# Kernel tuning notes

Hardware: AMD Instinct MI355X
Metric: run time of the kernel (lower is better)

Reference implementation:

```python
import jax, jax.numpy as jnp
import numpy as np

N_HEAD = 16
G_HEADS = 2
D_HEAD = 64
D_MODEL = 1024
HEAD_RATIO = N_HEAD // G_HEADS  # 8
QK_DIM = G_HEADS * D_HEAD       # 128
SCALE = 1.0 / D_HEAD ** 0.5
LN_EPS = 1e-5


def _rel_shift(x):
    # x: [qlen, rlen, B, n] -- Transformer-XL relative shift
    q, r = x.shape[0], x.shape[1]
    x_pad = jnp.pad(x, ((0, 0), (1, 0), (0, 0), (0, 0)))      # [q, r+1, B, n]
    x_pad = x_pad.reshape(r + 1, q, *x.shape[2:])[1:]          # drop first row
    return x_pad.reshape(q, r, *x.shape[2:])


def setup_inputs() -> dict:
    key = jax.random.key(0)
    ks = jax.random.split(key, 9)
    qlen, bsz, levels = 1024, 4, 3
    w = jax.random.normal(ks[0], (qlen, bsz, D_MODEL), jnp.float32)
    r = jax.random.normal(ks[1], (qlen, D_MODEL), jnp.float32)
    r_w_bias = jax.random.normal(ks[2], (G_HEADS, D_HEAD), jnp.float32) * 0.02
    r_r_bias = jax.random.normal(ks[3], (G_HEADS, D_HEAD), jnp.float32) * 0.02
    masks = jax.random.uniform(ks[4], (qlen, qlen, levels), jnp.float32)
    W_qkv = jax.random.normal(ks[5], (2 * QK_DIM + N_HEAD * D_HEAD, D_MODEL), jnp.float32) * 0.02
    W_r = jax.random.normal(ks[6], (QK_DIM, D_MODEL), jnp.float32) * 0.02
    mask_proj = jnp.ones((levels, N_HEAD), jnp.float32)
    W_o = jax.random.normal(ks[7], (D_MODEL, N_HEAD * D_HEAD), jnp.float32) * 0.02
    ln_gamma = jnp.ones((D_MODEL,), jnp.float32)
    ln_beta = jnp.zeros((D_MODEL,), jnp.float32)
    return dict(w=w, r=r, r_w_bias=r_w_bias, r_r_bias=r_r_bias, masks=masks,
                W_qkv=W_qkv, W_r=W_r, mask_proj=mask_proj, W_o=W_o,
                ln_gamma=ln_gamma, ln_beta=ln_beta)


def reference(w, r, r_w_bias, r_r_bias, masks, W_qkv, W_r, mask_proj, W_o, ln_gamma, ln_beta):
    qlen, bsz, _ = w.shape
    rlen = r.shape[0]
    N = qlen  # no mems: klen == qlen == rlen

    w_heads = w @ W_qkv.T                                   # [q, B, 1280]
    r_head_k = (r @ W_r.T).reshape(rlen, G_HEADS, D_HEAD)   # [r, gH, d]
    w_head_q = w_heads[..., :QK_DIM].reshape(qlen, bsz, G_HEADS, D_HEAD)
    w_head_k = w_heads[..., QK_DIM:2 * QK_DIM].reshape(qlen, bsz, G_HEADS, D_HEAD)
    w_head_v = w_heads[..., 2 * QK_DIM:].reshape(qlen, bsz, N_HEAD, D_HEAD)

    AC = jnp.einsum('ibnd,jbnd->ijbn', w_head_q + r_w_bias, w_head_k)
    BD = jnp.einsum('ibnd,jnd->ijbn', w_head_q + r_r_bias, r_head_k)
    BD = _rel_shift(BD)
    attn_score = (AC + BD) * SCALE                           # [N, N, B, gH]

    # per-head mask mixing ('full' projection)
    attn = jnp.transpose(attn_score, (2, 3, 0, 1))           # [B, gH, N, N]
    mw = (masks @ mask_proj).reshape(N, N, G_HEADS, HEAD_RATIO)
    mw = jnp.transpose(mw, (2, 0, 1, 3))                     # [gH, N, N, hr]
    attn = attn[..., None] * mw[None]                        # [B, gH, N, N, hr]
    attn = jnp.transpose(attn, (0, 1, 4, 2, 3)).reshape(bsz, N_HEAD, N, N)
    attn_score = jnp.transpose(attn, (2, 3, 0, 1))           # [N, N, B, H]

    attn_prob = jax.nn.softmax(attn_score, axis=1)
    attn_vec = jnp.einsum('ijbn,jbnd->ibnd', attn_prob, w_head_v)
    attn_vec = attn_vec.reshape(qlen, bsz, N_HEAD * D_HEAD)
    attn_out = attn_vec @ W_o.T                              # [q, B, d_model]

    # post-LN residual
    x = w + attn_out
    mu = jnp.mean(x, axis=-1, keepdims=True)
    var = jnp.mean((x - mu) ** 2, axis=-1, keepdims=True)
    return (x - mu) * jax.lax.rsqrt(var + LN_EPS) * ln_gamma + ln_beta
```

## Files before the change

### kernel.cpp

```cpp
#include <hip/hip_runtime.h>
#include <cstddef>
#include <cstdint>

#define QLEN   1024
#define SCALE  0.125f
#define LN_EPS 1e-5f
#define DMODEL 1024

typedef __bf16 bf16x8 __attribute__((ext_vector_type(8)));
typedef __bf16 bf16x4 __attribute__((ext_vector_type(4)));
typedef float  f32x4  __attribute__((ext_vector_type(4)));

__device__ __forceinline__ void load16_lds(const void* g, void* l) {
  __builtin_amdgcn_global_load_lds(
      (const __attribute__((address_space(1))) unsigned int*)g,
      (__attribute__((address_space(3))) unsigned int*)l, 16, 0, 0);
}

__device__ __forceinline__ void bar_lds() {
  asm volatile("s_waitcnt lgkmcnt(0)" ::: "memory");
  __builtin_amdgcn_s_barrier();
  asm volatile("" ::: "memory");
}

__global__ __launch_bounds__(256) void cast_all(
    const float* __restrict__ w, __bf16* __restrict__ w_bf,
    const float* __restrict__ Wqkv, __bf16* __restrict__ Wqkv_bf,
    const float* __restrict__ r, __bf16* __restrict__ r_bf,
    const float* __restrict__ Wr, __bf16* __restrict__ Wr_bf,
    const float* __restrict__ Wo, __bf16* __restrict__ Wo_bf)
{
  int blk = blockIdx.x;
  const float* in; __bf16* out;
  if (blk < 2048)      { in = w;    out = w_bf;    }
  else if (blk < 2688) { blk -= 2048; in = Wqkv; out = Wqkv_bf; }
  else if (blk < 3200) { blk -= 2688; in = r;    out = r_bf;    }
  else if (blk < 3264) { blk -= 3200; in = Wr;   out = Wr_bf;   }
  else                 { blk -= 3264; in = Wo;   out = Wo_bf;   }
  const size_t i = ((size_t)blk * 256 + threadIdx.x) * 8;
  const float4 a = *(const float4*)&in[i];
  const float4 b = *(const float4*)&in[i + 4];
  bf16x8 o;
  o[0] = (__bf16)a.x; o[1] = (__bf16)a.y; o[2] = (__bf16)a.z; o[3] = (__bf16)a.w;
  o[4] = (__bf16)b.x; o[5] = (__bf16)b.y; o[6] = (__bf16)b.z; o[7] = (__bf16)b.w;
  *(bf16x8*)&out[i] = o;
}

__global__ __launch_bounds__(256) void gemm_proj(
    const __bf16* __restrict__ w_bf, const __bf16* __restrict__ Wqkv_bf,
    const __bf16* __restrict__ r_bf, const __bf16* __restrict__ Wr_bf,
    const float* __restrict__ rwb, const float* __restrict__ rrb,
    __bf16* __restrict__ Qw, __bf16* __restrict__ Qr,
    __bf16* __restrict__ Kb, __bf16* __restrict__ Vt,
    __bf16* __restrict__ Rb)
{
  __shared__ __bf16 Asl[128 * 64];
  __shared__ __bf16 Bsl[64 * 64];
  const int blk = blockIdx.x;
  const bool isR = blk >= 640;
  const __bf16 *A, *B;
  int m0, n0;
  if (!isR) { A = w_bf; B = Wqkv_bf; n0 = (blk % 20) * 64; m0 = (blk / 20) * 128; }
  else      { const int k = blk - 640; A = r_bf; B = Wr_bf;
              n0 = (k % 2) * 64; m0 = (k / 2) * 128; }

  const int tid = threadIdx.x, lane = tid & 63, wv = tid >> 6;
  const int lr = lane & 15, kq = lane >> 4;
  const int s = lane & 7, ar = lane >> 3;

  f32x4 acc[2][4];
#pragma unroll
  for (int mt = 0; mt < 2; ++mt)
#pragma unroll
    for (int nt = 0; nt < 4; ++nt)
      acc[mt][nt] = (f32x4){0.f, 0.f, 0.f, 0.f};

  for (int k0 = 0; k0 < 1024; k0 += 64) {
#pragma unroll
    for (int p = 0; p < 4; ++p) {
      const int row = wv * 32 + p * 8 + ar;
      const int gc = (s - (row & 7)) & 7;
      load16_lds(A + (size_t)(m0 + row) * 1024 + k0 + gc * 8,
                 &Asl[row * 64 + s * 8]);
    }
#pragma unroll
    for (int p = 0; p < 2; ++p) {
      const int row = wv * 16 + p * 8 + ar;
      const int gc = (s - (row & 7)) & 7;
      load16_lds(B + (size_t)(n0 + row) * 1024 + k0 + gc * 8,
                 &Bsl[row * 64 + s * 8]);
    }
    __syncthreads();
#pragma unroll
    for (int ks = 0; ks < 2; ++ks) {
      const int c = ks * 4 + kq;
      bf16x8 af[2], bfr[4];
#pragma unroll
      for (int mt = 0; mt < 2; ++mt) {
        const int row = wv * 32 + mt * 16 + lr;
        af[mt] = *(const bf16x8*)&Asl[row * 64 + ((c + (row & 7)) & 7) * 8];
      }
#pragma unroll
      for (int nt = 0; nt < 4; ++nt) {
        const int row = nt * 16 + lr;
        bfr[nt] = *(const bf16x8*)&Bsl[row * 64 + ((c + (row & 7)) & 7) * 8];
      }
#pragma unroll
      for (int mt = 0; mt < 2; ++mt)
#pragma unroll
        for (int nt = 0; nt < 4; ++nt)
          acc[mt][nt] = __builtin_amdgcn_mfma_f32_16x16x32_bf16(
              af[mt], bfr[nt], acc[mt][nt], 0, 0, 0);
    }
    __syncthreads();
  }

#pragma unroll
  for (int mt = 0; mt < 2; ++mt) {
    const int row0 = m0 + wv * 32 + mt * 16 + kq * 4;
#pragma unroll
    for (int nt = 0; nt < 4; ++nt) {
      const int gcol = n0 + nt * 16 + lr;
      const f32x4 c = acc[mt][nt];
      if (isR) {
        const int g = gcol >> 6, d = gcol & 63;
#pragma unroll
        for (int reg = 0; reg < 4; ++reg)
          Rb[(size_t)g * 65536 + (size_t)(row0 + reg) * 64 + d] = (__bf16)c[reg];
      } else if (gcol < 128) {
        const int g = gcol >> 6, d = gcol & 63;
        const float bw = rwb[gcol], br = rrb[gcol];
#pragma unroll
        for (int reg = 0; reg < 4; ++reg) {
          const int row = row0 + reg, i = row >> 2, b = row & 3;
          const size_t o = (size_t)(b * 2 + g) * 65536 + (size_t)i * 64 + d;
          Qw[o] = (__bf16)(c[reg] + bw);
          Qr[o] = (__bf16)(c[reg] + br);
        }
      } else if (gcol < 256) {
        const int lc = gcol - 128, g = lc >> 6, d = lc & 63;
#pragma unroll
        for (int reg = 0; reg < 4; ++reg) {
          const int row = row0 + reg, i = row >> 2, b = row & 3;
          Kb[(size_t)(b * 2 + g) * 65536 + (size_t)i * 64 + d] = (__bf16)c[reg];
        }
      } else {
        const int lc = gcol - 256, h = lc >> 6, d = lc & 63;
#pragma unroll
        for (int reg = 0; reg < 4; ++reg) {
          const int row = row0 + reg, i = row >> 2, b = row & 3;
          Vt[((size_t)((b * 16 + h) * 64 + d)) * 1024 + i] = (__bf16)c[reg];
        }
      }
    }
  }
}

__global__ __launch_bounds__(256) void gemm_wo(
    const __bf16* __restrict__ A, const __bf16* __restrict__ B,
    float* __restrict__ C0, float* __restrict__ C1)
{
  __shared__ __bf16 Asl[128 * 64];
  __shared__ __bf16 Bsl[64 * 64];
  const int m0 = blockIdx.y * 128, n0 = blockIdx.x * 64;
  const int kh = blockIdx.z;
  float* __restrict__ C = kh ? C1 : C0;
  const int tid = threadIdx.x, lane = tid & 63, wv = tid >> 6;
  const int lr = lane & 15, kq = lane >> 4;
  const int s = lane & 7, ar = lane >> 3;
  const int kbase = kh * 512;

  f32x4 acc[2][4];
#pragma unroll
  for (int mt = 0; mt < 2; ++mt)
#pragma unroll
    for (int nt = 0; nt < 4; ++nt)
      acc[mt][nt] = (f32x4){0.f, 0.f, 0.f, 0.f};

  for (int k0 = 0; k0 < 512; k0 += 64) {
#pragma unroll
    for (int p = 0; p < 4; ++p) {
      const int row = wv * 32 + p * 8 + ar;
      const int gc = (s - (row & 7)) & 7;
      load16_lds(A + (size_t)(m0 + row) * 1024 + kbase + k0 + gc * 8,
                 &Asl[row * 64 + s * 8]);
    }
#pragma unroll
    for (int p = 0; p < 2; ++p) {
      const int row = wv * 16 + p * 8 + ar;
      const int gc = (s - (row & 7)) & 7;
      load16_lds(B + (size_t)(n0 + row) * 1024 + kbase + k0 + gc * 8,
                 &Bsl[row * 64 + s * 8]);
    }
    __syncthreads();
#pragma unroll
    for (int ks = 0; ks < 2; ++ks) {
      const int c = ks * 4 + kq;
      bf16x8 af[2], bfr[4];
#pragma unroll
      for (int mt = 0; mt < 2; ++mt) {
        const int row = wv * 32 + mt * 16 + lr;
        af[mt] = *(const bf16x8*)&Asl[row * 64 + ((c + (row & 7)) & 7) * 8];
      }
#pragma unroll
      for (int nt = 0; nt < 4; ++nt) {
        const int row = nt * 16 + lr;
        bfr[nt] = *(const bf16x8*)&Bsl[row * 64 + ((c + (row & 7)) & 7) * 8];
      }
#pragma unroll
      for (int mt = 0; mt < 2; ++mt)
#pragma unroll
        for (int nt = 0; nt < 4; ++nt)
          acc[mt][nt] = __builtin_amdgcn_mfma_f32_16x16x32_bf16(
              af[mt], bfr[nt], acc[mt][nt], 0, 0, 0);
    }
    __syncthreads();
  }

#pragma unroll
  for (int mt = 0; mt < 2; ++mt) {
    const int row0 = m0 + wv * 32 + mt * 16 + kq * 4;
#pragma unroll
    for (int nt = 0; nt < 4; ++nt) {
      const int col = n0 + nt * 16 + lr;
      const f32x4 c = acc[mt][nt];
#pragma unroll
      for (int reg = 0; reg < 4; ++reg)
        C[(size_t)(row0 + reg) * 1024 + col] = c[reg];
    }
  }
}

__global__ __launch_bounds__(256) void gemm64_bf16(
    const __bf16* __restrict__ Qw, const __bf16* __restrict__ Qr,
    const __bf16* __restrict__ Kb, const __bf16* __restrict__ Rb,
    __bf16* __restrict__ AC, __bf16* __restrict__ BDo)
{
  __shared__ __bf16 Asl[128 * 64];
  __shared__ __bf16 Bsl[128 * 64];
  const int tid = threadIdx.x, lane = tid & 63, wv = tid >> 6;
  const int which = blockIdx.z & 1, bat = blockIdx.z >> 1;
  const int m0 = blockIdx.y * 128, n0 = blockIdx.x * 128;
  const __bf16* Ap = (which ? Qr : Qw) + (size_t)bat * 65536;
  const __bf16* Bp = which ? (Rb + (size_t)(bat & 1) * 65536)
                           : (Kb + (size_t)bat * 65536);
  __bf16* Cp = (which ? BDo : AC) + (size_t)bat * 1048576;

#pragma unroll
  for (int p = 0; p < 4; ++p) {
    const int row = wv * 32 + p * 8 + (lane >> 3);
    const int s = lane & 7;
    const int gc = (s - (row & 7)) & 7;
    load16_lds(Ap + (size_t)(m0 + row) * 64 + gc * 8, &Asl[row * 64 + s * 8]);
    load16_lds(Bp + (size_t)(n0 + row) * 64 + gc * 8, &Bsl[row * 64 + s * 8]);
  }
  __syncthreads();

  const int lr = lane & 15, kq = lane >> 4;
  const int wm = (wv >> 1) * 64, wn = (wv & 1) * 64;
  f32x4 acc[4][4];
#pragma unroll
  for (int mt = 0; mt < 4; ++mt)
#pragma unroll
    for (int nt = 0; nt < 4; ++nt)
      acc[mt][nt] = (f32x4){0.f, 0.f, 0.f, 0.f};

#pragma unroll
  for (int ks = 0; ks < 2; ++ks) {
    const int c = ks * 4 + kq;
    bf16x8 af[4], bfr[4];
#pragma unroll
    for (int mt = 0; mt < 4; ++mt) {
      const int row = wm + mt * 16 + lr;
      af[mt] = *(const bf16x8*)&Asl[row * 64 + ((c + (row & 7)) & 7) * 8];
    }
#pragma unroll
    for (int nt = 0; nt < 4; ++nt) {
      const int row = wn + nt * 16 + lr;
      bfr[nt] = *(const bf16x8*)&Bsl[row * 64 + ((c + (row & 7)) & 7) * 8];
    }
#pragma unroll
    for (int mt = 0; mt < 4; ++mt)
#pragma unroll
      for (int nt = 0; nt < 4; ++nt)
        acc[mt][nt] = __builtin_amdgcn_mfma_f32_16x16x32_bf16(
            af[mt], bfr[nt], acc[mt][nt], 0, 0, 0);
  }

#pragma unroll
  for (int mt = 0; mt < 4; ++mt) {
    const int row0 = m0 + wm + mt * 16 + kq * 4;
#pragma unroll
    for (int nt = 0; nt < 4; ++nt) {
      const int col = n0 + wn + nt * 16 + lr;
      const f32x4 cc = acc[mt][nt];
      if (which) {
#pragma unroll
        for (int reg = 0; reg < 4; ++reg) {
          const int k = row0 + reg;
          const int thr = 1023 - k;
          if (col >= thr) {
            Cp[(size_t)k * 1024 + (col - thr)] = (__bf16)cc[reg];
            if (col == thr && k < 1023)
              Cp[(size_t)k * 1024 + (k + 1)] = (__bf16)0.f;
          } else if (k > 0) {
            Cp[(size_t)(k - 1) * 1024 + (col + k + 1)] = (__bf16)cc[reg];
          }
        }
      } else {
#pragma unroll
        for (int reg = 0; reg < 4; ++reg)
          Cp[(size_t)(row0 + reg) * 1024 + col] = (__bf16)cc[reg];
      }
    }
  }
}

__global__ __launch_bounds__(256) void prep3(
    const __bf16* __restrict__ AC, const __bf16* __restrict__ BDs,
    __bf16* __restrict__ Tg,
    const float* __restrict__ masks, const float* __restrict__ mproj,
    __bf16* __restrict__ Mh)
{
  const int tid = threadIdx.x;
  if (blockIdx.x < 2048) {
    const size_t base = (size_t)blockIdx.x * 4096 + (size_t)tid * 16;
    const bf16x8 a0 = *(const bf16x8*)&AC[base];
    const bf16x8 a1 = *(const bf16x8*)&AC[base + 8];
    const bf16x8 b0 = *(const bf16x8*)&BDs[base];
    const bf16x8 b1 = *(const bf16x8*)&BDs[base + 8];
    bf16x8 o0, o1;
#pragma unroll
    for (int k = 0; k < 8; ++k) {
      o0[k] = (__bf16)(((float)a0[k] + (float)b0[k]) * SCALE);
      o1[k] = (__bf16)(((float)a1[k] + (float)b1[k]) * SCALE);
    }
    *(bf16x8*)&Tg[base] = o0;
    *(bf16x8*)&Tg[base + 8] = o1;
  } else {
    const int blk = blockIdx.x - 2048;
    const size_t ij0 = ((size_t)blk * 256 + tid) * 4;
    const float4 a = *(const float4*)&masks[ij0 * 3];
    const float4 b = *(const float4*)&masks[ij0 * 3 + 4];
    const float4 c = *(const float4*)&masks[ij0 * 3 + 8];
    const float m0[4] = {a.x, a.w, b.z, c.y};
    const float m1[4] = {a.y, b.x, b.w, c.z};
    const float m2[4] = {a.z, b.y, c.x, c.w};
#pragma unroll
    for (int h = 0; h < 16; ++h) {
      const float p0 = mproj[h], p1 = mproj[16 + h], p2 = mproj[32 + h];
      bf16x4 o;
#pragma unroll
      for (int k = 0; k < 4; ++k)
        o[k] = (__bf16)(m0[k] * p0 + m1[k] * p1 + m2[k] * p2);
      *(bf16x4*)&Mh[(size_t)h * 1048576 + ij0] = o;
    }
  }
}

__global__ __launch_bounds__(256, 6) void attn10(
    const __bf16* __restrict__ Tg, const __bf16* __restrict__ Mh,
    const __bf16* __restrict__ Vt, __bf16* __restrict__ av, const int b0)
{
  __shared__ __bf16 P[2][32 * 128];
  __shared__ float rinvS[32];
  const int tid = threadIdx.x;
  const int i0 = blockIdx.x * 32;
  const int h = blockIdx.y, b = blockIdx.z + b0;
  const int g = h >> 3;
  const size_t bg = (size_t)(b * 2 + g);
  const int r = tid >> 3, li = tid & 7;
  const __bf16* Trow = Tg + bg * 1048576 + (size_t)(i0 + r) * 1024 + li * 8;
  const __bf16* Mrow = Mh + (size_t)h * 1048576 + (size_t)(i0 + r) * 1024 + li * 8;

  const int lane = tid & 63, wv = tid >> 6;
  const int m = lane & 15, kq = lane >> 4;
  const __bf16* vbase = Vt + ((size_t)((b * 16 + h) * 64 + wv * 16 + m)) * 1024 + kq * 8;

  float sum = 0.f;
  f32x4 acc[2][2];
#pragma unroll
  for (int mt = 0; mt < 2; ++mt)
#pragma unroll
    for (int u = 0; u < 2; ++u)
      acc[mt][u] = (f32x4){0.f, 0.f, 0.f, 0.f};

  bf16x8 t[2], mk[2], v[4];
#pragma unroll
  for (int q = 0; q < 2; ++q) {
    t[q]  = *(const bf16x8*)&Trow[q * 64];
    mk[q] = *(const bf16x8*)&Mrow[q * 64];
  }

  for (int ch = 0; ch < 8; ++ch) {
    const int cb = ch & 1;
#pragma unroll
    for (int ks = 0; ks < 4; ++ks)
      v[ks] = *(const bf16x8*)&vbase[(ch * 4 + ks) * 32];
#pragma unroll
    for (int q = 0; q < 2; ++q) {
      bf16x8 p8;
      float s0 = 0.f;
#pragma unroll
      for (int k = 0; k < 8; ++k) {
        const float e = __expf((float)t[q][k] * (float)mk[q][k]);
        s0 += e;
        p8[k] = (__bf16)e;
      }
      sum += s0;
      const int slot = (q * 8 + li) ^ (r & 7);
      *(bf16x8*)&P[cb][r * 128 + slot * 8] = p8;
    }
    if (ch < 7) {
#pragma unroll
      for (int q = 0; q < 2; ++q) {
        t[q]  = *(const bf16x8*)&Trow[(ch + 1) * 128 + q * 64];
        mk[q] = *(const bf16x8*)&Mrow[(ch + 1) * 128 + q * 64];
      }
    }
    bar_lds();
    __builtin_amdgcn_s_setprio(1);
#pragma unroll
    for (int ks = 0; ks < 4; ++ks) {
      const int c = ks * 4 + kq;
#pragma unroll
      for (int mt = 0; mt < 2; ++mt) {
        const int R = mt * 16 + m;
        const bf16x8 a = *(const bf16x8*)&P[cb][R * 128 + ((c ^ (R & 7)) << 3)];
        acc[mt][ks & 1] = __builtin_amdgcn_mfma_f32_16x16x32_bf16(
            a, v[ks], acc[mt][ks & 1], 0, 0, 0);
      }
    }
    __builtin_amdgcn_s_setprio(0);
  }

  sum += __shfl_xor(sum, 1);
  sum += __shfl_xor(sum, 2);
  sum += __shfl_xor(sum, 4);
  if (li == 0) rinvS[r] = 1.f / sum;
  __syncthreads();

#pragma unroll
  for (int mt = 0; mt < 2; ++mt) {
    const f32x4 accf = acc[mt][0] + acc[mt][1];
#pragma unroll
    for (int reg = 0; reg < 4; ++reg) {
      const int row = mt * 16 + kq * 4 + reg;
      av[((size_t)(i0 + row) * 4 + b) * 1024 + h * 64 + wv * 16 + m] =
          (__bf16)(accf[reg] * rinvS[row]);
    }
  }
}

__global__ __launch_bounds__(256) void ln_kernel(
    const float* __restrict__ w, const float* __restrict__ ao0,
    const float* __restrict__ ao1,
    const float* __restrict__ gamma, const float* __restrict__ beta,
    float* __restrict__ out)
{
  const int tid = threadIdx.x;
  const int lane = tid & 63, wv = tid >> 6;
  const size_t base = (size_t)blockIdx.x * DMODEL + tid * 4;
  __shared__ float red[8];
  const float4 xw = *(const float4*)&w[base];
  const float4 xa = *(const float4*)&ao0[base];
  const float4 xb = *(const float4*)&ao1[base];
  float x[4] = {xw.x + xa.x + xb.x, xw.y + xa.y + xb.y,
                xw.z + xa.z + xb.z, xw.w + xa.w + xb.w};
  float s = (x[0] + x[1]) + (x[2] + x[3]);
  s += __shfl_xor(s, 1);  s += __shfl_xor(s, 2);  s += __shfl_xor(s, 4);
  s += __shfl_xor(s, 8);  s += __shfl_xor(s, 16); s += __shfl_xor(s, 32);
  if (lane == 0) red[wv] = s;
  __syncthreads();
  const float mu = (red[0] + red[1] + red[2] + red[3]) * (1.f / DMODEL);
  float s2 = 0.f;
#pragma unroll
  for (int p = 0; p < 4; ++p) { const float t = x[p] - mu; s2 += t * t; }
  s2 += __shfl_xor(s2, 1);  s2 += __shfl_xor(s2, 2);  s2 += __shfl_xor(s2, 4);
  s2 += __shfl_xor(s2, 8);  s2 += __shfl_xor(s2, 16); s2 += __shfl_xor(s2, 32);
  if (lane == 0) red[4 + wv] = s2;
  __syncthreads();
  const float rs = rsqrtf((red[4] + red[5] + red[6] + red[7]) * (1.f / DMODEL) + LN_EPS);
  const float4 g4 = *(const float4*)&gamma[tid * 4];
  const float4 b4 = *(const float4*)&beta[tid * 4];
  float4 o;
  o.x = (x[0] - mu) * rs * g4.x + b4.x;
  o.y = (x[1] - mu) * rs * g4.y + b4.y;
  o.z = (x[2] - mu) * rs * g4.z + b4.z;
  o.w = (x[3] - mu) * rs * g4.w + b4.w;
  *(float4*)&out[base] = o;
}

extern "C" void kernel_launch(void* const* d_in, const int* in_sizes, int n_in,
                              void* d_out, int out_size, void* d_ws, size_t ws_size,
                              hipStream_t stream)
{
  const float* w     = (const float*)d_in[0];
  const float* r     = (const float*)d_in[1];
  const float* rwb   = (const float*)d_in[2];
  const float* rrb   = (const float*)d_in[3];
  const float* masks = (const float*)d_in[4];
  const float* Wqkv  = (const float*)d_in[5];
  const float* Wr    = (const float*)d_in[6];
  const float* mproj = (const float*)d_in[7];
  const float* Wo    = (const float*)d_in[8];
  const float* gam   = (const float*)d_in[9];
  const float* bet   = (const float*)d_in[10];
  float* out = (float*)d_out;

  float* ws = (float*)d_ws;
  __bf16* w_bf    = (__bf16*)(ws);
  __bf16* Wqkv_bf = (__bf16*)(ws + 2097152);
  __bf16* r_bf    = (__bf16*)(ws + 2752512);
  __bf16* Wr_bf   = (__bf16*)(ws + 3276800);
  __bf16* Qw      = (__bf16*)(ws + 3342336);
  __bf16* Qr      = (__bf16*)(ws + 3604480);
  __bf16* Kb      = (__bf16*)(ws + 3866624);
  __bf16* Rb      = (__bf16*)(ws + 4128768);
  __bf16* Mh      = (__bf16*)(ws);
  __bf16* AC_bf   = (__bf16*)(ws + 8388608);
  float*  ao0     = ws + 8388608;
  __bf16* BD_bf   = (__bf16*)(ws + 12582912);
  float*  ao1     = ws + 12582912;
  __bf16* Tg      = (__bf16*)(ws + 16777216);
  __bf16* Vt      = (__bf16*)(ws + 20971520);
  __bf16* av_bf   = (__bf16*)(ws + 23068672);
  __bf16* Wo_bf   = (__bf16*)(ws + 25165824);

  cast_all<<<3776, 256, 0, stream>>>(w, w_bf, Wqkv, Wqkv_bf, r, r_bf,
                                     Wr, Wr_bf, Wo, Wo_bf);
  gemm_proj<<<656, 256, 0, stream>>>(
      w_bf, Wqkv_bf, r_bf, Wr_bf, rwb, rrb, Qw, Qr, Kb, Vt, Rb);
  gemm64_bf16<<<dim3(8, 8, 16), 256, 0, stream>>>(Qw, Qr, Kb, Rb, AC_bf, BD_bf);
  prep3<<<3072, 256, 0, stream>>>(AC_bf, BD_bf, Tg, masks, mproj, Mh);
  attn10<<<dim3(32, 16, 2), 256, 0, stream>>>(Tg, Mh, Vt, av_bf, 0);
  attn10<<<dim3(32, 16, 2), 256, 0, stream>>>(Tg, Mh, Vt, av_bf, 2);
  gemm_wo<<<dim3(16, 32, 2), 256, 0, stream>>>(av_bf, Wo_bf, ao0, ao1);
  ln_kernel<<<4096, 256, 0, stream>>>(w, ao0, ao1, gam, bet, out);
}
```

Before: 232.7 us.

## Move mask mixing into cast kernel and double-buffer register prefetch in attention

New measurement: 247.9 us. 1.07x slower.

```diff
diff --git a/kernel.cpp b/kernel.cpp
--- a/kernel.cpp
+++ b/kernel.cpp
@@ -28,9 +28,31 @@
     const float* __restrict__ Wqkv, __bf16* __restrict__ Wqkv_bf,
     const float* __restrict__ r, __bf16* __restrict__ r_bf,
     const float* __restrict__ Wr, __bf16* __restrict__ Wr_bf,
-    const float* __restrict__ Wo, __bf16* __restrict__ Wo_bf)
+    const float* __restrict__ Wo, __bf16* __restrict__ Wo_bf,
+    const float* __restrict__ masks, const float* __restrict__ mproj,
+    __bf16* __restrict__ Mh)
 {
   int blk = blockIdx.x;
+  if (blk >= 3776) {
+    blk -= 3776;
+    const size_t ij0 = ((size_t)blk * 256 + threadIdx.x) * 4;
+    const float4 a = *(const float4*)&masks[ij0 * 3];
+    const float4 b = *(const float4*)&masks[ij0 * 3 + 4];
+    const float4 c = *(const float4*)&masks[ij0 * 3 + 8];
+    const float m0[4] = {a.x, a.w, b.z, c.y};
+    const float m1[4] = {a.y, b.x, b.w, c.z};
+    const float m2[4] = {a.z, b.y, c.x, c.w};
+#pragma unroll
+    for (int h = 0; h < 16; ++h) {
+      const float p0 = mproj[h], p1 = mproj[16 + h], p2 = mproj[32 + h];
+      bf16x4 o;
+#pragma unroll
+      for (int k = 0; k < 4; ++k)
+        o[k] = (__bf16)(m0[k] * p0 + m1[k] * p1 + m2[k] * p2);
+      *(bf16x4*)&Mh[(size_t)h * 1048576 + ij0] = o;
+    }
+    return;
+  }
   const float* in; __bf16* out;
   if (blk < 2048)      { in = w;    out = w_bf;    }
   else if (blk < 2688) { blk -= 2048; in = Wqkv; out = Wqkv_bf; }
@@ -316,49 +338,26 @@
   }
 }
 
-__global__ __launch_bounds__(256) void prep3(
+__global__ __launch_bounds__(256) void prep_T(
     const __bf16* __restrict__ AC, const __bf16* __restrict__ BDs,
-    __bf16* __restrict__ Tg,
-    const float* __restrict__ masks, const float* __restrict__ mproj,
-    __bf16* __restrict__ Mh)
-{
-  const int tid = threadIdx.x;
-  if (blockIdx.x < 2048) {
-    const size_t base = (size_t)blockIdx.x * 4096 + (size_t)tid * 16;
-    const bf16x8 a0 = *(const bf16x8*)&AC[base];
-    const bf16x8 a1 = *(const bf16x8*)&AC[base + 8];
-    const bf16x8 b0 = *(const bf16x8*)&BDs[base];
-    const bf16x8 b1 = *(const bf16x8*)&BDs[base + 8];
-    bf16x8 o0, o1;
-#pragma unroll
-    for (int k = 0; k < 8; ++k) {
-      o0[k] = (__bf16)(((float)a0[k] + (float)b0[k]) * SCALE);
-      o1[k] = (__bf16)(((float)a1[k] + (float)b1[k]) * SCALE);
-    }
-    *(bf16x8*)&Tg[base] = o0;
-    *(bf16x8*)&Tg[base + 8] = o1;
-  } else {
-    const int blk = blockIdx.x - 2048;
-    const size_t ij0 = ((size_t)blk * 256 + tid) * 4;
-    const float4 a = *(const float4*)&masks[ij0 * 3];
-    const float4 b = *(const float4*)&masks[ij0 * 3 + 4];
-    const float4 c = *(const float4*)&masks[ij0 * 3 + 8];
-    const float m0[4] = {a.x, a.w, b.z, c.y};
-    const float m1[4] = {a.y, b.x, b.w, c.z};
-    const float m2[4] = {a.z, b.y, c.x, c.w};
-#pragma unroll
-    for (int h = 0; h < 16; ++h) {
-      const float p0 = mproj[h], p1 = mproj[16 + h], p2 = mproj[32 + h];
-      bf16x4 o;
-#pragma unroll
-      for (int k = 0; k < 4; ++k)
-        o[k] = (__bf16)(m0[k] * p0 + m1[k] * p1 + m2[k] * p2);
-      *(bf16x4*)&Mh[(size_t)h * 1048576 + ij0] = o;
-    }
-  }
-}
-
-__global__ __launch_bounds__(256, 6) void attn10(
+    __bf16* __restrict__ Tg)
+{
+  const size_t base = (size_t)blockIdx.x * 4096 + (size_t)threadIdx.x * 16;
+  const bf16x8 a0 = *(const bf16x8*)&AC[base];
+  const bf16x8 a1 = *(const bf16x8*)&AC[base + 8];
+  const bf16x8 b0 = *(const bf16x8*)&BDs[base];
+  const bf16x8 b1 = *(const bf16x8*)&BDs[base + 8];
+  bf16x8 o0, o1;
+#pragma unroll
+  for (int k = 0; k < 8; ++k) {
+    o0[k] = (__bf16)(((float)a0[k] + (float)b0[k]) * SCALE);
+    o1[k] = (__bf16)(((float)a1[k] + (float)b1[k]) * SCALE);
+  }
+  *(bf16x8*)&Tg[base] = o0;
+  *(bf16x8*)&Tg[base + 8] = o1;
+}
+
+__global__ __launch_bounds__(256, 4) void attn11(
     const __bf16* __restrict__ Tg, const __bf16* __restrict__ Mh,
     const __bf16* __restrict__ Vt, __bf16* __restrict__ av, const int b0)
 {
@@ -385,38 +384,38 @@
     for (int u = 0; u < 2; ++u)
       acc[mt][u] = (f32x4){0.f, 0.f, 0.f, 0.f};
 
-  bf16x8 t[2], mk[2], v[4];
+  bf16x8 tA[2], mkA[2], vA[4], tB[2], mkB[2], vB[4];
 #pragma unroll
   for (int q = 0; q < 2; ++q) {
-    t[q]  = *(const bf16x8*)&Trow[q * 64];
-    mk[q] = *(const bf16x8*)&Mrow[q * 64];
-  }
-
-  for (int ch = 0; ch < 8; ++ch) {
-    const int cb = ch & 1;
+    tA[q]  = *(const bf16x8*)&Trow[q * 64];
+    mkA[q] = *(const bf16x8*)&Mrow[q * 64];
+  }
+#pragma unroll
+  for (int ks = 0; ks < 4; ++ks)
+    vA[ks] = *(const bf16x8*)&vbase[ks * 32];
+
+  for (int ch = 0; ch < 8; ch += 2) {
+#pragma unroll
+    for (int q = 0; q < 2; ++q) {
+      tB[q]  = *(const bf16x8*)&Trow[(ch + 1) * 128 + q * 64];
+      mkB[q] = *(const bf16x8*)&Mrow[(ch + 1) * 128 + q * 64];
+    }
 #pragma unroll
     for (int ks = 0; ks < 4; ++ks)
-      v[ks] = *(const bf16x8*)&vbase[(ch * 4 + ks) * 32];
+      vB[ks] = *(const bf16x8*)&vbase[((ch + 1) * 4 + ks) * 32];
 #pragma unroll
     for (int q = 0; q < 2; ++q) {
       bf16x8 p8;
       float s0 = 0.f;
 #pragma unroll
       for (int k = 0; k < 8; ++k) {
-        const float e = __expf((float)t[q][k] * (float)mk[q][k]);
+        const float e = __expf((float)tA[q][k] * (float)mkA[q][k]);
         s0 += e;
         p8[k] = (__bf16)e;
       }
       sum += s0;
       const int slot = (q * 8 + li) ^ (r & 7);
-      *(bf16x8*)&P[cb][r * 128 + slot * 8] = p8;
-    }
-    if (ch < 7) {
-#pragma unroll
-      for (int q = 0; q < 2; ++q) {
-        t[q]  = *(const bf16x8*)&Trow[(ch + 1) * 128 + q * 64];
-        mk[q] = *(const bf16x8*)&Mrow[(ch + 1) * 128 + q * 64];
-      }
+      *(bf16x8*)&P[0][r * 128 + slot * 8] = p8;
     }
     bar_lds();
     __builtin_amdgcn_s_setprio(1);
@@ -426,9 +425,48 @@
 #pragma unroll
       for (int mt = 0; mt < 2; ++mt) {
         const int R = mt * 16 + m;
-        const bf16x8 a = *(const bf16x8*)&P[cb][R * 128 + ((c ^ (R & 7)) << 3)];
+        const bf16x8 a = *(const bf16x8*)&P[0][R * 128 + ((c ^ (R & 7)) << 3)];
         acc[mt][ks & 1] = __builtin_amdgcn_mfma_f32_16x16x32_bf16(
-            a, v[ks], acc[mt][ks & 1], 0, 0, 0);
+            a, vA[ks], acc[mt][ks & 1], 0, 0, 0);
+      }
+    }
+    __builtin_amdgcn_s_setprio(0);
+
+    if (ch + 2 < 8) {
+#pragma unroll
+      for (int q = 0; q < 2; ++q) {
+        tA[q]  = *(const bf16x8*)&Trow[(ch + 2) * 128 + q * 64];
+        mkA[q] = *(const bf16x8*)&Mrow[(ch + 2) * 128 + q * 64];
+      }
+#pragma unroll
+      for (int ks = 0; ks < 4; ++ks)
+        vA[ks] = *(const bf16x8*)&vbase[((ch + 2) * 4 + ks) * 32];
+    }
+#pragma unroll
+    for (int q = 0; q < 2; ++q) {
+      bf16x8 p8;
+      float s0 = 0.f;
+#pragma unroll
+      for (int k = 0; k < 8; ++k) {
+        const float e = __expf((float)tB[q][k] * (float)mkB[q][k]);
+        s0 += e;
+        p8[k] = (__bf16)e;
+      }
+      sum += s0;
+      const int slot = (q * 8 + li) ^ (r & 7);
+      *(bf16x8*)&P[1][r * 128 + slot * 8] = p8;
+    }
+    bar_lds();
+    __builtin_amdgcn_s_setprio(1);
+#pragma unroll
+    for (int ks = 0; ks < 4; ++ks) {
+      const int c = ks * 4 + kq;
+#pragma unroll
+      for (int mt = 0; mt < 2; ++mt) {
+        const int R = mt * 16 + m;
+        const bf16x8 a = *(const bf16x8*)&P[1][R * 128 + ((c ^ (R & 7)) << 3)];
+        acc[mt][ks & 1] = __builtin_amdgcn_mfma_f32_16x16x32_bf16(
+            a, vB[ks], acc[mt][ks & 1], 0, 0, 0);
       }
     }
     __builtin_amdgcn_s_setprio(0);
@@ -517,7 +555,6 @@
   __bf16* Qr      = (__bf16*)(ws + 3604480);
   __bf16* Kb      = (__bf16*)(ws + 3866624);
   __bf16* Rb      = (__bf16*)(ws + 4128768);
-  __bf16* Mh      = (__bf16*)(ws);
   __bf16* AC_bf   = (__bf16*)(ws + 8388608);
   float*  ao0     = ws + 8388608;
   __bf16* BD_bf   = (__bf16*)(ws + 12582912);
@@ -526,15 +563,16 @@
   __bf16* Vt      = (__bf16*)(ws + 20971520);
   __bf16* av_bf   = (__bf16*)(ws + 23068672);
   __bf16* Wo_bf   = (__bf16*)(ws + 25165824);
-
-  cast_all<<<3776, 256, 0, stream>>>(w, w_bf, Wqkv, Wqkv_bf, r, r_bf,
-                                     Wr, Wr_bf, Wo, Wo_bf);
+  __bf16* Mh      = (__bf16*)(ws + 25690112);
+
+  cast_all<<<4800, 256, 0, stream>>>(w, w_bf, Wqkv, Wqkv_bf, r, r_bf,
+                                     Wr, Wr_bf, Wo, Wo_bf, masks, mproj, Mh);
   gemm_proj<<<656, 256, 0, stream>>>(
       w_bf, Wqkv_bf, r_bf, Wr_bf, rwb, rrb, Qw, Qr, Kb, Vt, Rb);
   gemm64_bf16<<<dim3(8, 8, 16), 256, 0, stream>>>(Qw, Qr, Kb, Rb, AC_bf, BD_bf);
-  prep3<<<3072, 256, 0, stream>>>(AC_bf, BD_bf, Tg, masks, mproj, Mh);
-  attn10<<<dim3(32, 16, 2), 256, 0, stream>>>(Tg, Mh, Vt, av_bf, 0);
-  attn10<<<dim3(32, 16, 2), 256, 0, stream>>>(Tg, Mh, Vt, av_bf, 2);
+  prep_T<<<2048, 256, 0, stream>>>(AC_bf, BD_bf, Tg);
+  attn11<<<dim3(32, 16, 2), 256, 0, stream>>>(Tg, Mh, Vt, av_bf, 0);
+  attn11<<<dim3(32, 16, 2), 256, 0, stream>>>(Tg, Mh, Vt, av_bf, 2);
   gemm_wo<<<dim3(16, 32, 2), 256, 0, stream>>>(av_bf, Wo_bf, ao0, ao1);
   ln_kernel<<<4096, 256, 0, stream>>>(w, ao0, ao1, gam, bet, out);
 }
```
